# Performance work log

Measured on AMD Instinct MI355X. Metric: run time of the kernel, lower is better.

The kernel has to match this reference:

```python
import jax, jax.numpy as jnp
import numpy as np

B, N, D_IN, D_HID, D_OUT = 64, 512, 512, 512, 512


def setup_inputs() -> dict:
    key = jax.random.key(0)
    ks = jax.random.split(key, 8)
    gain = 0.02  # xavier_normal_ gain used in reset_parameters_xavier

    def xavier(k, fan_in, fan_out):
        std = gain * np.sqrt(2.0 / (fan_in + fan_out))
        return jax.random.normal(k, (fan_in, fan_out), dtype=jnp.float32) * std

    return {
        "batch_graph": jax.random.normal(ks[0], (B, N, D_IN), dtype=jnp.float32),
        "adj": jax.random.uniform(ks[1], (B, N, N), dtype=jnp.float32),
        "W1": xavier(ks[2], D_IN, D_HID),
        "b1": jnp.zeros((D_HID,), dtype=jnp.float32),
        "W2": xavier(ks[3], D_HID, D_HID),
        "b2": jnp.zeros((D_HID,), dtype=jnp.float32),
        "W3": xavier(ks[4], D_HID, D_OUT),
        "b3": jnp.zeros((D_OUT,), dtype=jnp.float32),
    }


def _normalize_adj(adj):
    # rowsum^-0.5 with inf -> 0 (original: torch.pow then isinf mask)
    rowsum = adj.sum(axis=1)                       # [B, N] (sum over dim 1, as in torch)
    safe = jnp.where(rowsum == 0, 1.0, rowsum)
    r = jnp.where(rowsum == 0, 0.0, safe ** -0.5)  # [B, N]
    # (adj @ D)^T @ D = D @ adj^T @ D with D = diag(r)
    return r[:, :, None] * jnp.swapaxes(adj, 1, 2) * r[:, None, :]


def reference(batch_graph, adj, W1, b1, W2, b2, W3, b3):
    # Block-diagonal big_adj @ big_graph == per-graph batched matmul.
    A = _normalize_adj(adj)  # [B, N, N]

    def gc(x, W, b):
        # support = x @ W ; output = A @ support + b
        return jnp.einsum('bij,bjd->bid', A, x @ W) + b

    # dropout is identity in eval mode (deterministic reference)
    x = jax.nn.relu(gc(batch_graph, W1, b1))
    x = jax.nn.relu(gc(x, W2, b2))
    return gc(x, W3, b3)  # [B, N, D_OUT]
```

## Files before the change

kernel.cpp:

```cpp
#include <hip/hip_runtime.h>
#include <cstdint>
#include <cstddef>

typedef _Float16 f16;
typedef _Float16 f16x4 __attribute__((ext_vector_type(4)));
typedef _Float16 f16x8 __attribute__((ext_vector_type(8)));
typedef float    f32x4 __attribute__((ext_vector_type(4)));

#define NB 64
#define NN 262144

__device__ __forceinline__ void gload_lds16(const void* g, void* l) {
    __builtin_amdgcn_global_load_lds(
        (const __attribute__((address_space(1))) void*)g,
        (__attribute__((address_space(3))) void*)l, 16, 0, 0);
}

__global__ __launch_bounds__(256)
void k_aux(const float* __restrict__ X0, f16* __restrict__ X_h,
           const float* __restrict__ W1, const float* __restrict__ W2,
           const float* __restrict__ W3, f16* __restrict__ Wt,
           const float* __restrict__ adj, float* __restrict__ part) {
    __shared__ float t[64][65];
    const int bid = blockIdx.x, tid = threadIdx.x;

    {
        float4 v[8];
        #pragma unroll
        for (int s = 0; s < 4; ++s) {
            size_t i = (((size_t)(bid + 2048 * s)) * 256 + tid) * 8;
            v[2 * s]     = *(const float4*)(X0 + i);
            v[2 * s + 1] = *(const float4*)(X0 + i + 4);
        }
        #pragma unroll
        for (int s = 0; s < 4; ++s) {
            size_t i = (((size_t)(bid + 2048 * s)) * 256 + tid) * 8;
            f16x8 o;
            o[0] = (f16)v[2*s].x;   o[1] = (f16)v[2*s].y;
            o[2] = (f16)v[2*s].z;   o[3] = (f16)v[2*s].w;
            o[4] = (f16)v[2*s+1].x; o[5] = (f16)v[2*s+1].y;
            o[6] = (f16)v[2*s+1].z; o[7] = (f16)v[2*s+1].w;
            *(f16x8*)(X_h + i) = o;
        }
    }

    if (bid < 1024) {
        int b = bid >> 4;
        int rr0 = (bid & 15) * 32 + (tid >> 7) * 16;
        int c4 = (tid & 127) * 4;
        const float* ab = adj + (size_t)b * NN + (size_t)rr0 * 512 + c4;
        f32x4 s = {0.f, 0.f, 0.f, 0.f};
        #pragma unroll
        for (int i = 0; i < 16; ++i)
            s += *(const f32x4*)(ab + (size_t)i * 512);
        int ch2 = (bid & 15) * 2 + (tid >> 7);
        *(f32x4*)&part[((size_t)b * 32 + ch2) * 512 + c4] = s;
    } else if (bid < 1216) {
        int tt = bid - 1024;
        int z = tt >> 6, rem = tt & 63;
        const float* W = z == 0 ? W1 : (z == 1 ? W2 : W3);
        f16* out = Wt + (size_t)z * NN;
        int k0 = (rem >> 3) * 64, d0 = (rem & 7) * 64;
        int c = tid & 63, r4 = tid >> 6;
        #pragma unroll
        for (int s = 0; s < 16; ++s) {
            int rr = r4 + s * 4;
            t[rr][c] = W[(size_t)(k0 + rr) * 512 + d0 + c];
        }
        __syncthreads();
        int kq = (tid & 15) * 4;
        int db = tid >> 4;
        #pragma unroll
        for (int s = 0; s < 4; ++s) {
            int dd = db + s * 16;
            f16x4 o;
            #pragma unroll
            for (int q = 0; q < 4; ++q)
                o[q] = (f16)(64.f * t[kq + q][dd]);
            *(f16x4*)&out[(size_t)(d0 + dd) * 512 + k0 + kq] = o;
        }
    }
}

__global__ void k_makeA(const float* __restrict__ adj, const float* __restrict__ part,
                        f16* __restrict__ A_h) {
    __shared__ float t[64][68];
    __shared__ float ri_s[64], rj_s[64];
    const int tid = threadIdx.x;
    int b = blockIdx.z;
    int i0 = blockIdx.y * 64, j0 = blockIdx.x * 64;
    const float* ab = adj + (size_t)b * NN;
    int trow = tid >> 4;
    int tc4  = (tid & 15) * 4;
    #pragma unroll
    for (int s = 0; s < 4; ++s) {
        int rr = trow + s * 16;
        *(f32x4*)&t[rr][tc4] = *(const f32x4*)&ab[(size_t)(j0 + rr) * 512 + i0 + tc4];
    }
    if (tid < 128) {
        int col = tid < 64 ? i0 + tid : j0 + tid - 64;
        const float* p = part + (size_t)b * 32 * 512 + col;
        float s = 0.f;
        #pragma unroll
        for (int ch = 0; ch < 32; ++ch) s += p[ch * 512];
        float rv = (s > 0.f) ? rsqrtf(s) : 0.f;
        if (tid < 64) ri_s[tid] = rv;
        else          rj_s[tid - 64] = rv;
    }
    __syncthreads();
    f16* Ab = A_h + (size_t)b * NN;
    int jq = (tid & 15) * 4;
    int ib = tid >> 4;
    #pragma unroll
    for (int s = 0; s < 4; ++s) {
        int ii = ib + s * 16;
        float ri = 16.f * ri_s[ii];
        f16x4 o;
        #pragma unroll
        for (int q = 0; q < 4; ++q)
            o[q] = (f16)(ri * t[jq + q][ii] * rj_s[jq + q]);
        *(f16x4*)&Ab[(size_t)(i0 + ii) * 512 + j0 + jq] = o;
    }
}

template<bool BIAS, bool RELU, bool OUTF32>
__global__ __launch_bounds__(256, 2)
void gemm_tn_ct(const f16* __restrict__ P, size_t pstr,
                const f16* __restrict__ Qt, size_t qstr,
                void* __restrict__ Cout, size_t cstr,
                const float* __restrict__ bias, float iscale, float oscale) {
    __shared__ __align__(16) f16 Plds[2][8192];
    __shared__ __align__(16) f16 Qlds[2][8192];

    const int tid  = threadIdx.x;
    const int lane = tid & 63;
    const int wid  = tid >> 6;
    const int wm   = wid >> 1;
    const int wn   = wid & 1;

    const int wg  = blockIdx.x;
    const int swz = (wg & 7) * 128 + (wg >> 3);
    const int b   = swz >> 4;
    const int tt  = swz & 15;
    const int m0  = (tt >> 2) * 128;
    const int n0  = (tt & 3) * 128;

    const f16* Pb = P + (size_t)b * pstr;
    const f16* Qb = Qt + (size_t)b * qstr;

    const int srow = tid >> 3;
    const int sswz = (tid & 7) ^ (srow & 7);

    const int fr  = lane & 15;
    const int fs  = lane >> 4;
    const int fx  = fr & 7;

    auto stage = [&](const f16* __restrict__ Gb, int row0, f16* lds, int k0) {
        #pragma unroll
        for (int r = 0; r < 4; ++r) {
            const f16* src = Gb + (size_t)(row0 + r * 32 + srow) * 512 + k0 + sswz * 8;
            gload_lds16(src, lds + r * 2048 + tid * 8);
        }
    };

    f32x4 acc[4][4] = {};

    stage(Pb, m0, &Plds[0][0], 0);
    stage(Qb, n0, &Qlds[0][0], 0);

    for (int t = 0; t < 8; ++t) {
        const int nb = t & 1;
        if (t < 7) {
            stage(Pb, m0, &Plds[nb ^ 1][0], (t + 1) * 64);
            stage(Qb, n0, &Qlds[nb ^ 1][0], (t + 1) * 64);
            asm volatile("s_waitcnt vmcnt(8)" ::: "memory");
        } else {
            asm volatile("s_waitcnt vmcnt(0)" ::: "memory");
        }
        __builtin_amdgcn_s_barrier();

        const f16* Pl = &Plds[nb][0];
        const f16* Ql = &Qlds[nb][0];
        #pragma unroll
        for (int krep = 0; krep < 2; ++krep) {
            const int sp = ((fs + krep * 4) ^ fx) * 8;
            f16x8 af[4], bf[4];
            #pragma unroll
            for (int mi = 0; mi < 4; ++mi)
                af[mi] = *(const f16x8*)&Pl[(wm * 64 + mi * 16 + fr) * 64 + sp];
            #pragma unroll
            for (int ni = 0; ni < 4; ++ni)
                bf[ni] = *(const f16x8*)&Ql[(wn * 64 + ni * 16 + fr) * 64 + sp];
            __builtin_amdgcn_s_setprio(1);
            #pragma unroll
            for (int mi = 0; mi < 4; ++mi)
                #pragma unroll
                for (int ni = 0; ni < 4; ++ni)
                    acc[mi][ni] = __builtin_amdgcn_mfma_f32_16x16x32_f16(
                        af[mi], bf[ni], acc[mi][ni], 0, 0, 0);
            __builtin_amdgcn_s_setprio(0);
        }
        asm volatile("s_waitcnt lgkmcnt(0)" ::: "memory");
        __builtin_amdgcn_sched_barrier(0);
        __builtin_amdgcn_s_barrier();
    }

    const int cmb = (lane >> 4) * 4;
    #pragma unroll
    for (int mi = 0; mi < 4; ++mi) {
        #pragma unroll
        for (int ni = 0; ni < 4; ++ni) {
            const int n = n0 + wn * 64 + ni * 16 + fr;
            const int m = m0 + wm * 64 + mi * 16 + cmb;
            float v[4];
            #pragma unroll
            for (int q = 0; q < 4; ++q) {
                float x = acc[mi][ni][q] * iscale;
                if (BIAS) x += bias[m + q];
                if (RELU) x = fmaxf(x, 0.f);
                v[q] = x * oscale;
            }
            if (OUTF32) {
                float* Cb = (float*)Cout + (size_t)b * cstr;
                f32x4 o; o[0] = v[0]; o[1] = v[1]; o[2] = v[2]; o[3] = v[3];
                *(f32x4*)&Cb[(size_t)n * 512 + m] = o;
            } else {
                f16* Cb = (f16*)Cout + (size_t)b * cstr;
                f16x4 o; o[0] = (f16)v[0]; o[1] = (f16)v[1]; o[2] = (f16)v[2]; o[3] = (f16)v[3];
                *(f16x4*)&Cb[(size_t)n * 512 + m] = o;
            }
        }
    }
}

extern "C" void kernel_launch(void* const* d_in, const int* in_sizes, int n_in,
                              void* d_out, int out_size, void* d_ws, size_t ws_size,
                              hipStream_t stream) {
    const float* X0  = (const float*)d_in[0];
    const float* adj = (const float*)d_in[1];
    const float* W1  = (const float*)d_in[2];
    const float* b1  = (const float*)d_in[3];
    const float* W2  = (const float*)d_in[4];
    const float* b2  = (const float*)d_in[5];
    const float* W3  = (const float*)d_in[6];
    const float* b3  = (const float*)d_in[7];

    uint8_t* ws = (uint8_t*)d_ws;
    f16* Wt1 = (f16*)(ws + 131072);
    f16* Wt2 = Wt1 + NN;
    f16* Wt3 = Wt2 + NN;
    f16* A_h = (f16*)(ws + 131072 + (size_t)3 * NN * 2);
    f16* X_h = A_h + (size_t)NB * NN;
    f16* S_t = X_h + (size_t)NB * NN;
    float* part = (float*)S_t;

    k_aux  <<<dim3(2048),     dim3(256), 0, stream>>>(X0, X_h, W1, W2, W3, Wt1, adj, part);
    k_makeA<<<dim3(8, 8, NB), dim3(256), 0, stream>>>(adj, part, A_h);

    dim3 gg(1024), gb(256);
    gemm_tn_ct<false, false, false><<<gg, gb, 0, stream>>>(X_h, (size_t)NN, Wt1, (size_t)0,  S_t, (size_t)NN, nullptr, 1.f, 1.f / 64.f);
    gemm_tn_ct<true,  true,  false><<<gg, gb, 0, stream>>>(S_t, (size_t)NN, A_h, (size_t)NN, X_h, (size_t)NN, b1, 1.f / 16.f, 1.f);
    gemm_tn_ct<false, false, false><<<gg, gb, 0, stream>>>(X_h, (size_t)NN, Wt2, (size_t)0,  S_t, (size_t)NN, nullptr, 1.f, 4.f);
    gemm_tn_ct<true,  true,  false><<<gg, gb, 0, stream>>>(S_t, (size_t)NN, A_h, (size_t)NN, X_h, (size_t)NN, b2, 1.f / 4096.f, 256.f);
    gemm_tn_ct<false, false, false><<<gg, gb, 0, stream>>>(X_h, (size_t)NN, Wt3, (size_t)0,  S_t, (size_t)NN, nullptr, 1.f, 1.f / 64.f);
    gemm_tn_ct<true,  false, true ><<<gg, gb, 0, stream>>>(S_t, (size_t)NN, A_h, (size_t)NN, d_out, (size_t)NN, b3, 1.f / 4096.f, 1.f);
}
```

Before: 234.3 us.

## Fold degree normalization into GEMM epilogues and read adjacency once

The D^-1/2 row and column scalings move out of the materialized normalized adjacency and into the GEMM epilogues, applied as per-row or per-column factors through new template flags. Adjacency is now transposed and converted to fp16 in a single pass that also emits column partial sums. Previously it was read twice, once for row sums and once for building A. A small finalize kernel computes the rsqrt factors, and X conversion becomes a separate kernel. The risk is fp16 range, since raw adjacency and unnormalized products are rescaled with new constants, plus two extra launches.

```diff
diff --git a/kernel.cpp b/kernel.cpp
--- a/kernel.cpp
+++ b/kernel.cpp
@@ -16,48 +16,64 @@
         (__attribute__((address_space(3))) void*)l, 16, 0, 0);
 }
 
+__global__ void k_cvtX(const float* __restrict__ x, f16* __restrict__ xh) {
+    size_t i = ((size_t)blockIdx.x * 256 + threadIdx.x) * 8;
+    float4 v0 = *(const float4*)(x + i);
+    float4 v1 = *(const float4*)(x + i + 4);
+    f16x8 o;
+    o[0] = (f16)v0.x; o[1] = (f16)v0.y; o[2] = (f16)v0.z; o[3] = (f16)v0.w;
+    o[4] = (f16)v1.x; o[5] = (f16)v1.y; o[6] = (f16)v1.z; o[7] = (f16)v1.w;
+    *(f16x8*)(xh + i) = o;
+}
+
 __global__ __launch_bounds__(256)
-void k_aux(const float* __restrict__ X0, f16* __restrict__ X_h,
-           const float* __restrict__ W1, const float* __restrict__ W2,
-           const float* __restrict__ W3, f16* __restrict__ Wt,
-           const float* __restrict__ adj, float* __restrict__ part) {
-    __shared__ float t[64][65];
+void k_prep(const float* __restrict__ adj, f16* __restrict__ A_raw,
+            float* __restrict__ part,
+            const float* __restrict__ W1, const float* __restrict__ W2,
+            const float* __restrict__ W3, f16* __restrict__ Wt) {
+    __shared__ float t[64][68];
+    __shared__ float red[4][64];
     const int bid = blockIdx.x, tid = threadIdx.x;
-
-    {
-        float4 v[8];
+    if (bid < 4096) {
+        const int xcd = bid & 7, loc = bid >> 3;
+        const int b = xcd * 8 + (loc >> 6);
+        const int tile = loc & 63;
+        const int i0 = (tile >> 3) * 64, j0 = (tile & 7) * 64;
+        const int jt = tile & 7;
+        const float* ab = adj + (size_t)b * NN;
+        int trow = tid >> 4;
+        int tc4  = (tid & 15) * 4;
         #pragma unroll
         for (int s = 0; s < 4; ++s) {
-            size_t i = (((size_t)(bid + 2048 * s)) * 256 + tid) * 8;
-            v[2 * s]     = *(const float4*)(X0 + i);
-            v[2 * s + 1] = *(const float4*)(X0 + i + 4);
-        }
+            int rr = trow + s * 16;
+            *(f32x4*)&t[rr][tc4] = *(const f32x4*)&ab[(size_t)(j0 + rr) * 512 + i0 + tc4];
+        }
+        __syncthreads();
+        {
+            int c = tid & 63, g = tid >> 6;
+            float sg = 0.f;
+            #pragma unroll
+            for (int s = 0; s < 16; ++s) sg += t[g * 16 + s][c];
+            red[g][c] = sg;
+        }
+        f16* Ab = A_raw + (size_t)b * NN;
+        int jq = (tid & 15) * 4;
+        int ib = tid >> 4;
         #pragma unroll
         for (int s = 0; s < 4; ++s) {
-            size_t i = (((size_t)(bid + 2048 * s)) * 256 + tid) * 8;
-            f16x8 o;
-            o[0] = (f16)v[2*s].x;   o[1] = (f16)v[2*s].y;
-            o[2] = (f16)v[2*s].z;   o[3] = (f16)v[2*s].w;
-            o[4] = (f16)v[2*s+1].x; o[5] = (f16)v[2*s+1].y;
-            o[6] = (f16)v[2*s+1].z; o[7] = (f16)v[2*s+1].w;
-            *(f16x8*)(X_h + i) = o;
-        }
-    }
-
-    if (bid < 1024) {
-        int b = bid >> 4;
-        int rr0 = (bid & 15) * 32 + (tid >> 7) * 16;
-        int c4 = (tid & 127) * 4;
-        const float* ab = adj + (size_t)b * NN + (size_t)rr0 * 512 + c4;
-        f32x4 s = {0.f, 0.f, 0.f, 0.f};
-        #pragma unroll
-        for (int i = 0; i < 16; ++i)
-            s += *(const f32x4*)(ab + (size_t)i * 512);
-        int ch2 = (bid & 15) * 2 + (tid >> 7);
-        *(f32x4*)&part[((size_t)b * 32 + ch2) * 512 + c4] = s;
-    } else if (bid < 1216) {
-        int tt = bid - 1024;
-        int z = tt >> 6, rem = tt & 63;
+            int ii = ib + s * 16;
+            f16x4 o;
+            #pragma unroll
+            for (int q = 0; q < 4; ++q) o[q] = (f16)t[jq + q][ii];
+            *(f16x4*)&Ab[(size_t)(i0 + ii) * 512 + j0 + jq] = o;
+        }
+        __syncthreads();
+        if (tid < 64)
+            part[((size_t)b * 8 + jt) * 512 + i0 + tid] =
+                red[0][tid] + red[1][tid] + red[2][tid] + red[3][tid];
+    } else {
+        int cb = bid - 4096;
+        int z = cb >> 6, rem = cb & 63;
         const float* W = z == 0 ? W1 : (z == 1 ? W2 : W3);
         f16* out = Wt + (size_t)z * NN;
         int k0 = (rem >> 3) * 64, d0 = (rem & 7) * 64;
@@ -82,53 +98,23 @@
     }
 }
 
-__global__ void k_makeA(const float* __restrict__ adj, const float* __restrict__ part,
-                        f16* __restrict__ A_h) {
-    __shared__ float t[64][68];
-    __shared__ float ri_s[64], rj_s[64];
-    const int tid = threadIdx.x;
-    int b = blockIdx.z;
-    int i0 = blockIdx.y * 64, j0 = blockIdx.x * 64;
-    const float* ab = adj + (size_t)b * NN;
-    int trow = tid >> 4;
-    int tc4  = (tid & 15) * 4;
+__global__ void k_fin(const float* __restrict__ part, float* __restrict__ r) {
+    int idx = blockIdx.x * 256 + threadIdx.x;
+    int b = idx >> 9, n = idx & 511;
+    const float* p = part + (size_t)b * 8 * 512 + n;
+    float s = 0.f;
     #pragma unroll
-    for (int s = 0; s < 4; ++s) {
-        int rr = trow + s * 16;
-        *(f32x4*)&t[rr][tc4] = *(const f32x4*)&ab[(size_t)(j0 + rr) * 512 + i0 + tc4];
-    }
-    if (tid < 128) {
-        int col = tid < 64 ? i0 + tid : j0 + tid - 64;
-        const float* p = part + (size_t)b * 32 * 512 + col;
-        float s = 0.f;
-        #pragma unroll
-        for (int ch = 0; ch < 32; ++ch) s += p[ch * 512];
-        float rv = (s > 0.f) ? rsqrtf(s) : 0.f;
-        if (tid < 64) ri_s[tid] = rv;
-        else          rj_s[tid - 64] = rv;
-    }
-    __syncthreads();
-    f16* Ab = A_h + (size_t)b * NN;
-    int jq = (tid & 15) * 4;
-    int ib = tid >> 4;
-    #pragma unroll
-    for (int s = 0; s < 4; ++s) {
-        int ii = ib + s * 16;
-        float ri = 16.f * ri_s[ii];
-        f16x4 o;
-        #pragma unroll
-        for (int q = 0; q < 4; ++q)
-            o[q] = (f16)(ri * t[jq + q][ii] * rj_s[jq + q]);
-        *(f16x4*)&Ab[(size_t)(i0 + ii) * 512 + j0 + jq] = o;
-    }
-}
-
-template<bool BIAS, bool RELU, bool OUTF32>
+    for (int jt = 0; jt < 8; ++jt) s += p[jt * 512];
+    r[idx] = (s > 0.f) ? rsqrtf(s) : 0.f;
+}
+
+template<bool BIAS, bool RELU, bool OUTF32, bool RM, bool RN>
 __global__ __launch_bounds__(256, 2)
 void gemm_tn_ct(const f16* __restrict__ P, size_t pstr,
                 const f16* __restrict__ Qt, size_t qstr,
                 void* __restrict__ Cout, size_t cstr,
-                const float* __restrict__ bias, float iscale, float oscale) {
+                const float* __restrict__ bias, const float* __restrict__ rbuf,
+                float iscale, float oscale) {
     __shared__ __align__(16) f16 Plds[2][8192];
     __shared__ __align__(16) f16 Qlds[2][8192];
 
@@ -147,6 +133,7 @@
 
     const f16* Pb = P + (size_t)b * pstr;
     const f16* Qb = Qt + (size_t)b * qstr;
+    const float* rs = rbuf + (size_t)b * 512;
 
     const int srow = tid >> 3;
     const int sswz = (tid & 7) ^ (srow & 7);
@@ -206,6 +193,18 @@
     }
 
     const int cmb = (lane >> 4) * 4;
+    f32x4 rm4[4];
+    float rn1[4];
+    if (RM) {
+        #pragma unroll
+        for (int mi = 0; mi < 4; ++mi)
+            rm4[mi] = *(const f32x4*)&rs[m0 + wm * 64 + mi * 16 + cmb];
+    }
+    if (RN) {
+        #pragma unroll
+        for (int ni = 0; ni < 4; ++ni)
+            rn1[ni] = rs[n0 + wn * 64 + ni * 16 + fr];
+    }
     #pragma unroll
     for (int mi = 0; mi < 4; ++mi) {
         #pragma unroll
@@ -216,6 +215,8 @@
             #pragma unroll
             for (int q = 0; q < 4; ++q) {
                 float x = acc[mi][ni][q] * iscale;
+                if (RM) x *= rm4[mi][q];
+                if (RN) x *= rn1[ni];
                 if (BIAS) x += bias[m + q];
                 if (RELU) x = fmaxf(x, 0.f);
                 v[q] = x * oscale;
@@ -246,22 +247,24 @@
     const float* b3  = (const float*)d_in[7];
 
     uint8_t* ws = (uint8_t*)d_ws;
+    float* rbuf = (float*)ws;
     f16* Wt1 = (f16*)(ws + 131072);
     f16* Wt2 = Wt1 + NN;
     f16* Wt3 = Wt2 + NN;
-    f16* A_h = (f16*)(ws + 131072 + (size_t)3 * NN * 2);
-    f16* X_h = A_h + (size_t)NB * NN;
-    f16* S_t = X_h + (size_t)NB * NN;
+    f16* A_raw = (f16*)(ws + 131072 + (size_t)3 * NN * 2);
+    f16* Xa  = A_raw + (size_t)NB * NN;
+    f16* S_t = Xa + (size_t)NB * NN;
     float* part = (float*)S_t;
 
-    k_aux  <<<dim3(2048),     dim3(256), 0, stream>>>(X0, X_h, W1, W2, W3, Wt1, adj, part);
-    k_makeA<<<dim3(8, 8, NB), dim3(256), 0, stream>>>(adj, part, A_h);
+    k_prep<<<dim3(4288), dim3(256), 0, stream>>>(adj, A_raw, part, W1, W2, W3, Wt1);
+    k_cvtX<<<dim3(8192), dim3(256), 0, stream>>>(X0, Xa);
+    k_fin <<<dim3(128),  dim3(256), 0, stream>>>(part, rbuf);
 
     dim3 gg(1024), gb(256);
-    gemm_tn_ct<false, false, false><<<gg, gb, 0, stream>>>(X_h, (size_t)NN, Wt1, (size_t)0,  S_t, (size_t)NN, nullptr, 1.f, 1.f / 64.f);
-    gemm_tn_ct<true,  true,  false><<<gg, gb, 0, stream>>>(S_t, (size_t)NN, A_h, (size_t)NN, X_h, (size_t)NN, b1, 1.f / 16.f, 1.f);
-    gemm_tn_ct<false, false, false><<<gg, gb, 0, stream>>>(X_h, (size_t)NN, Wt2, (size_t)0,  S_t, (size_t)NN, nullptr, 1.f, 4.f);
-    gemm_tn_ct<true,  true,  false><<<gg, gb, 0, stream>>>(S_t, (size_t)NN, A_h, (size_t)NN, X_h, (size_t)NN, b2, 1.f / 4096.f, 256.f);
-    gemm_tn_ct<false, false, false><<<gg, gb, 0, stream>>>(X_h, (size_t)NN, Wt3, (size_t)0,  S_t, (size_t)NN, nullptr, 1.f, 1.f / 64.f);
-    gemm_tn_ct<true,  false, true ><<<gg, gb, 0, stream>>>(S_t, (size_t)NN, A_h, (size_t)NN, d_out, (size_t)NN, b3, 1.f / 4096.f, 1.f);
-}
+    gemm_tn_ct<false, false, false, true,  false><<<gg, gb, 0, stream>>>(Xa,  (size_t)NN, Wt1, (size_t)0,  S_t, (size_t)NN, nullptr, rbuf, 4.f, 1.f);
+    gemm_tn_ct<true,  true,  false, false, true ><<<gg, gb, 0, stream>>>(S_t, (size_t)NN, A_raw, (size_t)NN, Xa, (size_t)NN, b1, rbuf, 1.f / 256.f, 256.f);
+    gemm_tn_ct<false, false, false, true,  false><<<gg, gb, 0, stream>>>(Xa,  (size_t)NN, Wt2, (size_t)0,  S_t, (size_t)NN, nullptr, rbuf, 16.f, 1.f);
+    gemm_tn_ct<true,  true,  false, false, true ><<<gg, gb, 0, stream>>>(S_t, (size_t)NN, A_raw, (size_t)NN, Xa, (size_t)NN, b2, rbuf, 1.f / 262144.f, 256.f);
+    gemm_tn_ct<false, false, false, true,  false><<<gg, gb, 0, stream>>>(Xa,  (size_t)NN, Wt3, (size_t)0,  S_t, (size_t)NN, nullptr, rbuf, 16.f, 1.f);
+    gemm_tn_ct<true,  false, true,  false, true ><<<gg, gb, 0, stream>>>(S_t, (size_t)NN, A_raw, (size_t)NN, d_out, (size_t)NN, b3, rbuf, 1.f / 262144.f, 1.f);
+}
```

New measurement: 219.6 us. 1.07x faster.
